# Optimization experiments

Measured on AMD Instinct MI355X. Metric: run time of the kernel, lower is better.

Reference implementation:

```python
import jax, jax.numpy as jnp
import numpy as np

HN, ND, STRIDE, ESTRIDE = 10, 40, 3, 3  # hidden_node, ndim, stride, encode_stride


def _build_graphs():
    # Dense aggregation matrices A[dst, src] equivalent to the module's fixed
    # edge lists (scatter-add of src features into dst). Graph is tiny (10/40
    # nodes) and identical across the batch, so dense matmul is the efficient
    # exact form of the gather->scatter-add.
    w = np.float32(np.exp(-(1.0 / STRIDE) ** 2))
    A_pred = np.zeros((HN, HN), np.float32)
    for j in range(HN):
        A_pred[j, j] += 1.0                      # edge [j, j], weight 1
        for dj in range(1, STRIDE - 1):          # dj = 1 only
            A_pred[(j - dj) % HN, j] += w        # edge [j, j-dj]
            A_pred[(j + dj) % HN, j] += w        # edge [j, j+dj]
    A_enc = np.zeros((HN, ND), np.float32)
    A_dec = np.zeros((ND, HN), np.float32)
    for j in range(HN):
        cg = (j * ND // HN) % ND                 # center_grid = 4j
        for i in range(cg - ESTRIDE, cg + ESTRIDE):
            A_enc[j, i % ND] += 1.0              # grid i -> hidden j
            A_dec[i % ND, j] += 1.0              # hidden j -> grid i
    return jnp.asarray(A_enc), jnp.asarray(A_pred), jnp.asarray(A_dec)

A_ENC, A_PRED, A_DEC = _build_graphs()


def setup_inputs() -> dict:
    key = jax.random.key(0)
    ks = jax.random.split(key, 12)
    B, HF = 524288, 8
    s = 0.3  # modest weight scale
    return {
        "x": jax.random.normal(ks[0], (B, ND), jnp.float32),
        "z": jax.random.uniform(ks[1], (B, HN, HF), dtype=jnp.float32),
        "y": jax.random.uniform(ks[2], (B, ND, 1), dtype=jnp.float32),
        "enc_rel_w": jax.random.normal(ks[3], (HF, 1), jnp.float32) * s,
        "enc_rel_b": jax.random.normal(ks[4], (HF,), jnp.float32) * s,
        "enc_root_w": jax.random.normal(ks[5], (HF, HF), jnp.float32) * s,
        "pred_rel_w": jax.random.normal(ks[6], (HF, HF), jnp.float32) * s,
        "pred_rel_b": jax.random.normal(ks[7], (HF,), jnp.float32) * s,
        "pred_root_w": jax.random.normal(ks[8], (HF, HF), jnp.float32) * s,
        "dec_rel_w": jax.random.normal(ks[9], (1, HF), jnp.float32) * s,
        "dec_rel_b": jax.random.normal(ks[10], (1,), jnp.float32) * s,
        "dec_root_w": jax.random.normal(ks[11], (1, 1), jnp.float32) * s,
    }


def reference(x, z, y, enc_rel_w, enc_rel_b, enc_root_w,
              pred_rel_w, pred_rel_b, pred_root_w,
              dec_rel_w, dec_rel_b, dec_root_w):
    xb = x[..., None]  # [B, 40, 1]
    # encoder GraphConv((1, 8) -> 8): lin_rel(agg(x_src)) + lin_root(z)
    agg = jnp.einsum('ds,bsf->bdf', A_ENC, xb)                 # [B, 10, 1]
    z1 = jax.nn.relu(agg @ enc_rel_w.T + enc_rel_b + z @ enc_root_w.T)
    # predictor GraphConv(8 -> 8) with edge weights folded into A_PRED
    agg2 = jnp.einsum('ds,bsf->bdf', A_PRED, z1)               # [B, 10, 8]
    z2 = jax.nn.relu(agg2 @ pred_rel_w.T + pred_rel_b + z1 @ pred_root_w.T)
    # decoder GraphConv((8, 1) -> 1)
    agg3 = jnp.einsum('ds,bsf->bdf', A_DEC, z2)                # [B, 40, 8]
    out = agg3 @ dec_rel_w.T + dec_rel_b + y @ dec_root_w.T   # [B, 40, 1]
    return out[..., 0]                                         # [B, 40]
```

## Files before the change

### kernel.cpp

```cpp
#include <hip/hip_runtime.h>


#define HN 10
#define ND 40
#define HF 8
#define TPB 256
#define WLEN 64
#define ROW4 11

__global__ __launch_bounds__(TPB) void gnn_kernel(
    const float* __restrict__ x,
    const float* __restrict__ z,
    const float* __restrict__ y,
    const float* __restrict__ enc_rel_w,
    const float* __restrict__ enc_rel_b,
    const float* __restrict__ enc_root_w,
    const float* __restrict__ pred_rel_w,
    const float* __restrict__ pred_rel_b,
    const float* __restrict__ pred_root_w,
    const float* __restrict__ dec_rel_w,
    const float* __restrict__ dec_rel_b,
    const float* __restrict__ dec_root_w,
    float* __restrict__ out,
    int B)
{
    __shared__ float4 lds4[TPB * ROW4];
    const int t    = threadIdx.x;
    const int lane = t & 63;
    const int wv   = t >> 6;
    const long long wbase = (long long)blockIdx.x * TPB + wv * WLEN;
    float4* wl = lds4 + wv * (WLEN * ROW4);

    const float w = 0.8948393168143698f;

    const float4* xg = (const float4*)(x + wbase * ND);
    #pragma unroll
    for (int k = 0; k < 10; ++k) {
        int i = lane + WLEN * k;
        int e = i / 10, q = i - e * 10;
        wl[e * ROW4 + q] = xg[i];
    }
    asm volatile("s_waitcnt lgkmcnt(0)" ::: "memory");
    __builtin_amdgcn_sched_barrier(0);

    float agg[HN];
    {
        float xv[ND];
        #pragma unroll
        for (int k = 0; k < 10; ++k) {
            float4 v = wl[lane * ROW4 + k];
            xv[4*k+0] = v.x; xv[4*k+1] = v.y; xv[4*k+2] = v.z; xv[4*k+3] = v.w;
        }
        agg[0] = xv[37] + xv[38] + xv[39] + xv[0] + xv[1] + xv[2];
        #pragma unroll
        for (int j = 1; j < HN; ++j)
            agg[j] = xv[4*j-3] + xv[4*j-2] + xv[4*j-1] + xv[4*j] + xv[4*j+1] + xv[4*j+2];
    }

    const float4* zrow = (const float4*)(z + (wbase + lane) * (HN * HF));
    float4 zA[10], zB[10];
    #pragma unroll
    for (int k = 0; k < 10; ++k) zA[k] = zrow[k];
    #pragma unroll
    for (int k = 0; k < 10; ++k) zB[k] = zrow[10 + k];

    auto enc_row = [&](float4 v0, float4 v1, int j, float (&r)[HF]) {
        float zr[HF] = {v0.x, v0.y, v0.z, v0.w, v1.x, v1.y, v1.z, v1.w};
        #pragma unroll
        for (int f = 0; f < HF; ++f) {
            float acc = agg[j] * enc_rel_w[f] + enc_rel_b[f];
            #pragma unroll
            for (int g = 0; g < HF; ++g)
                acc += zr[g] * enc_root_w[f * HF + g];
            r[f] = fmaxf(acc, 0.0f);
        }
    };

    auto emit = [&](const float (&rm)[HF], const float (&rc)[HF],
                    const float (&rp)[HF]) -> float {
        float a2[HF];
        #pragma unroll
        for (int f = 0; f < HF; ++f)
            a2[f] = rc[f] + w * (rm[f] + rp[f]);
        float s = 0.0f;
        #pragma unroll
        for (int f = 0; f < HF; ++f) {
            float acc = pred_rel_b[f];
            #pragma unroll
            for (int g = 0; g < HF; ++g)
                acc += a2[g] * pred_rel_w[f * HF + g];
            #pragma unroll
            for (int g = 0; g < HF; ++g)
                acc += rc[g] * pred_root_w[f * HF + g];
            s += fmaxf(acc, 0.0f) * dec_rel_w[f];
        }
        return s;
    };

    float rA[5][HF], rB[5][HF];
    #pragma unroll
    for (int jj = 0; jj < 5; ++jj) enc_row(zA[2*jj], zA[2*jj+1], jj, rA[jj]);
    #pragma unroll
    for (int jj = 0; jj < 5; ++jj) enc_row(zB[2*jj], zB[2*jj+1], 5 + jj, rB[jj]);

    float s2[HN];
    s2[1] = emit(rA[0], rA[1], rA[2]);
    s2[2] = emit(rA[1], rA[2], rA[3]);
    s2[3] = emit(rA[2], rA[3], rA[4]);
    s2[4] = emit(rA[3], rA[4], rB[0]);
    s2[5] = emit(rA[4], rB[0], rB[1]);
    s2[6] = emit(rB[0], rB[1], rB[2]);
    s2[7] = emit(rB[1], rB[2], rB[3]);
    s2[8] = emit(rB[2], rB[3], rB[4]);
    s2[9] = emit(rB[3], rB[4], rA[0]);
    s2[0] = emit(rB[4], rA[0], rA[1]);

    const float drb   = dec_rel_b[0];
    const float droot = dec_root_w[0];
    #pragma unroll
    for (int k = 0; k < 10; ++k) {
        const int k1 = (k + 1) % HN;
        const float pair = s2[k] + s2[k1] + drb;
        float4 vo;
        vo.x = s2[k] + drb;
        vo.y = pair;
        vo.z = pair;
        vo.w = s2[k1] + drb;
        wl[lane * ROW4 + k] = vo;
    }
    asm volatile("s_waitcnt lgkmcnt(0)" ::: "memory");
    __builtin_amdgcn_sched_barrier(0);

    const float4* yg = (const float4*)(y + wbase * ND);
    float4* og = (float4*)(out + wbase * ND);
    #pragma unroll
    for (int k = 0; k < 10; ++k) {
        int i = lane + WLEN * k;
        int e = i / 10, q = i - e * 10;
        float4 p = wl[e * ROW4 + q];
        float4 vy = yg[i];
        p.x += vy.x * droot;
        p.y += vy.y * droot;
        p.z += vy.z * droot;
        p.w += vy.w * droot;
        og[i] = p;
    }
}

extern "C" void kernel_launch(void* const* d_in, const int* in_sizes, int n_in,
                              void* d_out, int out_size, void* d_ws, size_t ws_size,
                              hipStream_t stream) {
    const float* x          = (const float*)d_in[0];
    const float* z          = (const float*)d_in[1];
    const float* y          = (const float*)d_in[2];
    const float* enc_rel_w  = (const float*)d_in[3];
    const float* enc_rel_b  = (const float*)d_in[4];
    const float* enc_root_w = (const float*)d_in[5];
    const float* pred_rel_w = (const float*)d_in[6];
    const float* pred_rel_b = (const float*)d_in[7];
    const float* pred_root_w= (const float*)d_in[8];
    const float* dec_rel_w  = (const float*)d_in[9];
    const float* dec_rel_b  = (const float*)d_in[10];
    const float* dec_root_w = (const float*)d_in[11];
    float* out = (float*)d_out;

    const int B = in_sizes[0] / ND;
    const int blocks = B / TPB;
    gnn_kernel<<<blocks, TPB, 0, stream>>>(
        x, z, y, enc_rel_w, enc_rel_b, enc_root_w,
        pred_rel_w, pred_rel_b, pred_root_w,
        dec_rel_w, dec_rel_b, dec_root_w, out, B);
}
```

Baseline: 412.6 us.

## Drop LDS staging and load x/y/out directly per thread

Removes the shared-memory transpose that coalesced the x loads and out/y stores. Each thread now reads its own 160-byte x and y rows and writes its out row directly with float4 accesses, and the z loads are split into two scoped halves to reduce register pressure. This drops LDS traffic and the wait barriers. In exchange, global accesses become strided per lane (160-byte stride), which can hurt coalescing efficiency.

```diff
diff --git a/kernel.cpp b/kernel.cpp
--- a/kernel.cpp
+++ b/kernel.cpp
@@ -5,8 +5,6 @@
 #define ND 40
 #define HF 8
 #define TPB 256
-#define WLEN 64
-#define ROW4 11
 
 __global__ __launch_bounds__(TPB) void gnn_kernel(
     const float* __restrict__ x,
@@ -24,54 +22,34 @@
     float* __restrict__ out,
     int B)
 {
-    __shared__ float4 lds4[TPB * ROW4];
-    const int t    = threadIdx.x;
-    const int lane = t & 63;
-    const int wv   = t >> 6;
-    const long long wbase = (long long)blockIdx.x * TPB + wv * WLEN;
-    float4* wl = lds4 + wv * (WLEN * ROW4);
+    const long long e = (long long)blockIdx.x * TPB + threadIdx.x;
 
     const float w = 0.8948393168143698f;
 
-    const float4* xg = (const float4*)(x + wbase * ND);
+    const float4* xr = (const float4*)(x + e * ND);
+    float xv[ND];
     #pragma unroll
     for (int k = 0; k < 10; ++k) {
-        int i = lane + WLEN * k;
-        int e = i / 10, q = i - e * 10;
-        wl[e * ROW4 + q] = xg[i];
+        float4 v = xr[k];
+        xv[4*k+0] = v.x; xv[4*k+1] = v.y; xv[4*k+2] = v.z; xv[4*k+3] = v.w;
     }
-    asm volatile("s_waitcnt lgkmcnt(0)" ::: "memory");
-    __builtin_amdgcn_sched_barrier(0);
 
     float agg[HN];
-    {
-        float xv[ND];
-        #pragma unroll
-        for (int k = 0; k < 10; ++k) {
-            float4 v = wl[lane * ROW4 + k];
-            xv[4*k+0] = v.x; xv[4*k+1] = v.y; xv[4*k+2] = v.z; xv[4*k+3] = v.w;
-        }
-        agg[0] = xv[37] + xv[38] + xv[39] + xv[0] + xv[1] + xv[2];
-        #pragma unroll
-        for (int j = 1; j < HN; ++j)
-            agg[j] = xv[4*j-3] + xv[4*j-2] + xv[4*j-1] + xv[4*j] + xv[4*j+1] + xv[4*j+2];
-    }
+    agg[0] = xv[37] + xv[38] + xv[39] + xv[0] + xv[1] + xv[2];
+    #pragma unroll
+    for (int j = 1; j < HN; ++j)
+        agg[j] = xv[4*j-3] + xv[4*j-2] + xv[4*j-1] + xv[4*j] + xv[4*j+1] + xv[4*j+2];
 
-    const float4* zrow = (const float4*)(z + (wbase + lane) * (HN * HF));
-    float4 zA[10], zB[10];
-    #pragma unroll
-    for (int k = 0; k < 10; ++k) zA[k] = zrow[k];
-    #pragma unroll
-    for (int k = 0; k < 10; ++k) zB[k] = zrow[10 + k];
+    const float4* zr = (const float4*)(z + e * (HN * HF));
 
     auto enc_row = [&](float4 v0, float4 v1, int j, float (&r)[HF]) {
-        float zr[HF] = {v0.x, v0.y, v0.z, v0.w, v1.x, v1.y, v1.z, v1.w};
+        float zrow[HF] = {v0.x, v0.y, v0.z, v0.w, v1.x, v1.y, v1.z, v1.w};
         #pragma unroll
         for (int f = 0; f < HF; ++f) {
             float acc = agg[j] * enc_rel_w[f] + enc_rel_b[f];
             #pragma unroll
             for (int g = 0; g < HF; ++g)
-                acc += zr[g] * enc_root_w[f * HF + g];
+                acc += zrow[g] * enc_root_w[f * HF + g];
             r[f] = fmaxf(acc, 0.0f);
         }
     };
@@ -98,10 +76,25 @@
     };
 
     float rA[5][HF], rB[5][HF];
+    {
+        float4 zA[10];
+        #pragma unroll
+        for (int k = 0; k < 10; ++k) zA[k] = zr[k];
+        #pragma unroll
+        for (int jj = 0; jj < 5; ++jj) enc_row(zA[2*jj], zA[2*jj+1], jj, rA[jj]);
+    }
+    {
+        float4 zB[10];
+        #pragma unroll
+        for (int k = 0; k < 10; ++k) zB[k] = zr[10 + k];
+        #pragma unroll
+        for (int jj = 0; jj < 5; ++jj) enc_row(zB[2*jj], zB[2*jj+1], 5 + jj, rB[jj]);
+    }
+
+    const float4* yr = (const float4*)(y + e * ND);
+    float4 yv[10];
     #pragma unroll
-    for (int jj = 0; jj < 5; ++jj) enc_row(zA[2*jj], zA[2*jj+1], jj, rA[jj]);
-    #pragma unroll
-    for (int jj = 0; jj < 5; ++jj) enc_row(zB[2*jj], zB[2*jj+1], 5 + jj, rB[jj]);
+    for (int k = 0; k < 10; ++k) yv[k] = yr[k];
 
     float s2[HN];
     s2[1] = emit(rA[0], rA[1], rA[2]);
@@ -117,33 +110,17 @@
 
     const float drb   = dec_rel_b[0];
     const float droot = dec_root_w[0];
+    float4* og = (float4*)(out + e * ND);
     #pragma unroll
     for (int k = 0; k < 10; ++k) {
         const int k1 = (k + 1) % HN;
         const float pair = s2[k] + s2[k1] + drb;
-        float4 vo;
-        vo.x = s2[k] + drb;
-        vo.y = pair;
-        vo.z = pair;
-        vo.w = s2[k1] + drb;
-        wl[lane * ROW4 + k] = vo;
-    }
-    asm volatile("s_waitcnt lgkmcnt(0)" ::: "memory");
-    __builtin_amdgcn_sched_barrier(0);
-
-    const float4* yg = (const float4*)(y + wbase * ND);
-    float4* og = (float4*)(out + wbase * ND);
-    #pragma unroll
-    for (int k = 0; k < 10; ++k) {
-        int i = lane + WLEN * k;
-        int e = i / 10, q = i - e * 10;
-        float4 p = wl[e * ROW4 + q];
-        float4 vy = yg[i];
-        p.x += vy.x * droot;
-        p.y += vy.y * droot;
-        p.z += vy.z * droot;
-        p.w += vy.w * droot;
-        og[i] = p;
+        float4 o;
+        o.x = (s2[k]  + drb) + yv[k].x * droot;
+        o.y = pair           + yv[k].y * droot;
+        o.z = pair           + yv[k].z * droot;
+        o.w = (s2[k1] + drb) + yv[k].w * droot;
+        og[k] = o;
     }
 }
 
```

Result: no change. 420.1 us (+1.8%).
